# Kernel optimization log

Measured on AMD Instinct MI355X. Metric: run time of the kernel, lower is better.

The kernel has to match this reference:

```python
import jax, jax.numpy as jnp
import numpy as np

N, E = 100000, 1600000
IN_C, HID, HEADS, OUT_C = 128, 32, 4, 2
NEG_SLOPE = 0.2


def _gat_layer(x, src, dst, W, a_src, a_dst, b, n_nodes, heads, c):
    # x: [N, F_in] -> h: [N, H, C]
    h = (x @ W).reshape(n_nodes, heads, c)
    alpha_s = jnp.sum(h * a_src, axis=-1)  # [N, H]
    alpha_d = jnp.sum(h * a_dst, axis=-1)  # [N, H]
    e = jax.nn.leaky_relu(alpha_s[src] + alpha_d[dst], NEG_SLOPE)  # [E, H]
    # segment softmax over incoming edges of each dst node
    m = jax.ops.segment_max(e, dst, num_segments=n_nodes)  # [N, H]
    ee = jnp.exp(e - m[dst])
    denom = jax.ops.segment_sum(ee, dst, num_segments=n_nodes)  # [N, H]
    alpha = ee / (denom[dst] + 1e-16)  # [E, H]
    out = jax.ops.segment_sum(h[src] * alpha[:, :, None], dst, num_segments=n_nodes)  # [N, H, C]
    return out.reshape(n_nodes, heads * c) + b


def _gat_forward(x, edge_index, W1, a_src1, a_dst1, b1, W2, a_src2, a_dst2, b2, Wfc, bfc):
    n = x.shape[0]
    loops = jnp.arange(n, dtype=edge_index.dtype)
    src = jnp.concatenate([edge_index[0], loops])  # PyG adds self-loops
    dst = jnp.concatenate([edge_index[1], loops])
    h = jax.nn.elu(_gat_layer(x, src, dst, W1, a_src1, a_dst1, b1, n, HEADS, HID))
    h = jax.nn.elu(_gat_layer(h, src, dst, W2, a_src2, a_dst2, b2, n, HEADS, HID))
    return h @ Wfc + bfc


def setup_inputs() -> dict:
    key = jax.random.key(0)
    ks = jax.random.split(key, 12)
    g = lambda k, shape, fan: jax.random.normal(k, shape, jnp.float32) * (1.0 / np.sqrt(fan))
    return {
        "x": jax.random.normal(ks[0], (N, IN_C), jnp.float32),
        "edge_index": jax.random.randint(ks[1], (2, E), 0, N, jnp.int64),
        "W1": g(ks[2], (IN_C, HEADS * HID), IN_C),
        "a_src1": g(ks[3], (HEADS, HID), HID),
        "a_dst1": g(ks[4], (HEADS, HID), HID),
        "b1": jnp.zeros((HEADS * HID,), jnp.float32),
        "W2": g(ks[5], (HEADS * HID, HEADS * HID), HEADS * HID),
        "a_src2": g(ks[6], (HEADS, HID), HID),
        "a_dst2": g(ks[7], (HEADS, HID), HID),
        "b2": jnp.zeros((HEADS * HID,), jnp.float32),
        "Wfc": g(ks[8], (HEADS * HID, OUT_C), HEADS * HID),
        "bfc": jnp.zeros((OUT_C,), jnp.float32),
    }


def reference(x, edge_index, W1, a_src1, a_dst1, b1, W2, a_src2, a_dst2, b2, Wfc, bfc):
    return _gat_forward(x, edge_index, W1, a_src1, a_dst1, b1, W2, a_src2, a_dst2, b2, Wfc, bfc)
```

## Files before the change

### kernel.cpp

```cpp
#include <hip/hip_runtime.h>
#include <hip/hip_fp16.h>
#include <math.h>

#define FEAT 128
#define NBLK 256
#define BSHIFT 8

typedef _Float16 f16x8 __attribute__((ext_vector_type(8)));
typedef float f32x4 __attribute__((ext_vector_type(4)));

__device__ __forceinline__ float eluf(float x) {
  return x > 0.0f ? x : (__expf(x) - 1.0f);
}


__global__ __launch_bounds__(256) void scan1_kernel(const int* __restrict__ cnt,
                                                    int* __restrict__ pre,
                                                    int* __restrict__ bsum, int n) {
  __shared__ int sd[256];
  const int t = threadIdx.x;
  const int idx = blockIdx.x * 1024 + t * 4;
  int4 v = make_int4(0, 0, 0, 0);
  if (idx + 3 < n) {
    v = *(const int4*)(cnt + idx);
  } else {
    if (idx < n)     v.x = cnt[idx];
    if (idx + 1 < n) v.y = cnt[idx + 1];
    if (idx + 2 < n) v.z = cnt[idx + 2];
    if (idx + 3 < n) v.w = cnt[idx + 3];
  }
  const int tsum = v.x + v.y + v.z + v.w;
  sd[t] = tsum;
  __syncthreads();
  for (int o = 1; o < 256; o <<= 1) {
    int x = (t >= o) ? sd[t - o] : 0;
    __syncthreads();
    sd[t] += x;
    __syncthreads();
  }
  const int excl = sd[t] - tsum;
  if (idx < n)     pre[idx]     = excl;
  if (idx + 1 < n) pre[idx + 1] = excl + v.x;
  if (idx + 2 < n) pre[idx + 2] = excl + v.x + v.y;
  if (idx + 3 < n) pre[idx + 3] = excl + v.x + v.y + v.z;
  if (t == 255) bsum[blockIdx.x] = sd[255];
}

__global__ __launch_bounds__(256) void scan2_kernel(int* __restrict__ bsum, int nb) {
  __shared__ int sd[256];
  const int t = threadIdx.x;
  int v = (t < nb) ? bsum[t] : 0;
  sd[t] = v;
  __syncthreads();
  for (int o = 1; o < 256; o <<= 1) {
    int x = (t >= o) ? sd[t - o] : 0;
    __syncthreads();
    sd[t] += x;
    __syncthreads();
  }
  if (t < nb) bsum[t] = sd[t] - v;
}

__global__ __launch_bounds__(256) void bucket_hist_kernel(
    const int* __restrict__ ei, int* __restrict__ gh,
    int E, int ET, int nbuck, int chunk) {
  __shared__ int h[512];
  const int t = threadIdx.x;
  const int b = blockIdx.x;
  h[t] = 0; h[t + 256] = 0;
  __syncthreads();
  const int lo = b * chunk;
  const int hi = min(lo + chunk, ET);
  for (int i = lo + t; i < hi; i += 256) {
    int d = (i < E) ? ei[E + i] : (i - E);
    atomicAdd(&h[d >> BSHIFT], 1);
  }
  __syncthreads();
  for (int k = t; k < nbuck; k += 256) gh[k * NBLK + b] = h[k];
}

__global__ __launch_bounds__(256) void bucket_scatter_kernel(
    const int* __restrict__ ei, const int* __restrict__ ghp,
    const int* __restrict__ bsum, unsigned* __restrict__ pairs,
    int E, int ET, int nbuck, int chunk) {
  __shared__ int cur[512];
  const int t = threadIdx.x;
  const int b = blockIdx.x;
  for (int k = t; k < nbuck; k += 256) {
    int idx = k * NBLK + b;
    cur[k] = ghp[idx] + bsum[idx >> 10];
  }
  __syncthreads();
  const int lo = b * chunk;
  const int hi = min(lo + chunk, ET);
  for (int i = lo + t; i < hi; i += 256) {
    int s, d;
    if (i < E) { s = ei[i]; d = ei[E + i]; } else { s = d = i - E; }
    int pos = atomicAdd(&cur[d >> BSHIFT], 1);
    pairs[pos] = ((unsigned)s << 8) | (unsigned)(d & 255);
  }
}

__global__ __launch_bounds__(256) void bucket_finalize_kernel(
    const unsigned* __restrict__ pairs, const int* __restrict__ ghp,
    const int* __restrict__ bsum, int* __restrict__ row_ptr,
    int* __restrict__ esrc, int N, int ET, int nbuck) {
  __shared__ int hist[256];
  __shared__ int cur[256];
  __shared__ int sd[256];
  const int t = threadIdx.x;
  const int k = blockIdx.x;
  const int node0 = k << BSHIFT;
  const int idx0 = k * NBLK;
  const int base = ghp[idx0] + bsum[idx0 >> 10];
  int end;
  if (k + 1 < nbuck) {
    const int idx1 = (k + 1) * NBLK;
    end = ghp[idx1] + bsum[idx1 >> 10];
  } else {
    end = ET;
  }
  hist[t] = 0;
  __syncthreads();
  for (int e = base + t; e < end; e += 256) {
    atomicAdd(&hist[pairs[e] & 255u], 1);
  }
  __syncthreads();
  const int v = hist[t];
  __syncthreads();
  sd[t] = v;
  __syncthreads();
  for (int o = 1; o < 256; o <<= 1) {
    int x = (t >= o) ? sd[t - o] : 0;
    __syncthreads();
    sd[t] += x;
    __syncthreads();
  }
  const int excl = sd[t] - v;
  if (node0 + t < N) row_ptr[node0 + t] = base + excl;
  cur[t] = excl;
  __syncthreads();
  for (int e = base + t; e < end; e += 256) {
    unsigned p = pairs[e];
    int pos = atomicAdd(&cur[p & 255u], 1);
    esrc[base + pos] = (int)(p >> 8);
  }
  if (k == 0 && t == 0) row_ptr[N] = ET;
}

__global__ __launch_bounds__(256) void pack_w_kernel(
    const float* __restrict__ W, const float* __restrict__ a_src,
    const float* __restrict__ a_dst, __half* __restrict__ frag) {
  const float LOG2E = 1.4426950408889634f;
  int tid = blockIdx.x * 256 + threadIdx.x;
  if (tid >= 4 * 9 * 64) return;
  int lane = tid & 63;
  int tile = (tid >> 6) % 9;
  int ks = tid / (9 * 64);
  int li = lane & 15, hi = lane >> 4;
  int col = tile * 16 + li;
  __half* dst = frag + (size_t)tid * 8;
  for (int i = 0; i < 8; ++i) {
    int k = ks * 32 + hi * 8 + i;
    float v = 0.f;
    if (col < 128) {
      v = W[k * 128 + col];
    } else if (col < 132) {
      int h = col - 128;
      float s = 0.f;
      for (int j = 0; j < 32; ++j) s += W[k * 128 + h * 32 + j] * a_src[h * 32 + j];
      v = s * LOG2E;
    } else if (col < 136) {
      int h = col - 132;
      float s = 0.f;
      for (int j = 0; j < 32; ++j) s += W[k * 128 + h * 32 + j] * a_dst[h * 32 + j];
      v = s * LOG2E;
    }
    dst[i] = __float2half(v);
  }
}

template <bool F32IN>
__device__ __forceinline__ f16x8 load_x(const void* in, int row, int ks, int hi) {
  f16x8 xf;
  if (F32IN) {
    const float* xp = (const float*)in + (size_t)row * FEAT + ks * 32 + hi * 8;
    float4 v0 = *(const float4*)xp;
    float4 v1 = *(const float4*)(xp + 4);
    xf[0] = (_Float16)v0.x; xf[1] = (_Float16)v0.y;
    xf[2] = (_Float16)v0.z; xf[3] = (_Float16)v0.w;
    xf[4] = (_Float16)v1.x; xf[5] = (_Float16)v1.y;
    xf[6] = (_Float16)v1.z; xf[7] = (_Float16)v1.w;
  } else {
    xf = *(const f16x8*)((const __half*)in + (size_t)row * FEAT + ks * 32 + hi * 8);
  }
  return xf;
}

template <bool F32IN>
__global__ __launch_bounds__(256) void gemm_mfma_kernel(
    const void* __restrict__ in, const __half* __restrict__ frag,
    __half* __restrict__ hout, float* __restrict__ as_out, float* __restrict__ ad_out,
    int nrows) {
  const int wv = (blockIdx.x * 256 + threadIdx.x) >> 6;
  const int lane = threadIdx.x & 63;
  const int li = lane & 15, hi = lane >> 4;
  const int ntiles = (nrows + 15) >> 4;
  const int t0 = wv * 2;
  if (t0 >= ntiles) return;

  int row0 = t0 * 16 + li;
  int row1 = row0 + 16;
  const bool v0 = row0 < nrows;
  const bool v1 = (t0 + 1 < ntiles) && (row1 < nrows);
  const int r0 = v0 ? row0 : nrows - 1;
  const int r1 = v1 ? row1 : nrows - 1;

  const f16x8* fragv = (const f16x8*)frag;

  f32x4 acc0[9], acc1[9];
#pragma unroll
  for (int t = 0; t < 9; ++t) {
    acc0[t] = (f32x4){0.f, 0.f, 0.f, 0.f};
    acc1[t] = (f32x4){0.f, 0.f, 0.f, 0.f};
  }

#pragma unroll
  for (int ks = 0; ks < 4; ++ks) {
    const f16x8 xf0 = load_x<F32IN>(in, r0, ks, hi);
    const f16x8 xf1 = load_x<F32IN>(in, r1, ks, hi);
#pragma unroll
    for (int t = 0; t < 9; ++t) {
      const f16x8 wf = fragv[(ks * 9 + t) * 64 + lane];
      acc0[t] = __builtin_amdgcn_mfma_f32_16x16x32_f16(wf, xf0, acc0[t], 0, 0, 0);
      acc1[t] = __builtin_amdgcn_mfma_f32_16x16x32_f16(wf, xf1, acc1[t], 0, 0, 0);
    }
  }

  if (v0) {
#pragma unroll
    for (int t = 0; t < 8; ++t) {
      union { __half2 h[2]; uint2 u; } pk;
      pk.h[0] = __floats2half2_rn(acc0[t][0], acc0[t][1]);
      pk.h[1] = __floats2half2_rn(acc0[t][2], acc0[t][3]);
      *(uint2*)(hout + (size_t)r0 * FEAT + t * 16 + hi * 4) = pk.u;
    }
    if (hi == 0) *(float4*)(as_out + r0 * 4) = make_float4(acc0[8][0], acc0[8][1], acc0[8][2], acc0[8][3]);
    if (hi == 1) *(float4*)(ad_out + r0 * 4) = make_float4(acc0[8][0], acc0[8][1], acc0[8][2], acc0[8][3]);
  }
  if (v1) {
#pragma unroll
    for (int t = 0; t < 8; ++t) {
      union { __half2 h[2]; uint2 u; } pk;
      pk.h[0] = __floats2half2_rn(acc1[t][0], acc1[t][1]);
      pk.h[1] = __floats2half2_rn(acc1[t][2], acc1[t][3]);
      *(uint2*)(hout + (size_t)r1 * FEAT + t * 16 + hi * 4) = pk.u;
    }
    if (hi == 0) *(float4*)(as_out + r1 * 4) = make_float4(acc1[8][0], acc1[8][1], acc1[8][2], acc1[8][3]);
    if (hi == 1) *(float4*)(ad_out + r1 * 4) = make_float4(acc1[8][0], acc1[8][1], acc1[8][2], acc1[8][3]);
  }
}

template <int MODE>
__global__ __launch_bounds__(256) void node_gat_kernel(
    const int* __restrict__ row_ptr, const int* __restrict__ esrc,
    const float* __restrict__ as_, const float* __restrict__ ad_,
    const __half2* __restrict__ h, const float* __restrict__ bias,
    __half2* __restrict__ out16, const float* __restrict__ fcw,
    const float* __restrict__ fcb, float* __restrict__ outf, int n) {
  const int wid = (blockIdx.x * 256 + threadIdx.x) >> 6;
  if (wid >= n) return;
  const int l = threadIdx.x & 63;
  const int begin = row_ptr[wid];
  const int end = row_ptr[wid + 1];
  const unsigned hd = (unsigned)(l >> 4);
  const float adv = ad_[(unsigned)wid * 4u + hd];
  const unsigned lofs = (unsigned)l;

  float2 a2 = make_float2(0.f, 0.f);
  float den = 0.f;
  int e = begin;

  for (; e + 7 < end; e += 8) {
    unsigned s[8];
#pragma unroll
    for (int i = 0; i < 8; ++i) s[i] = (unsigned)esrc[e + i];
    float as8[8];
#pragma unroll
    for (int i = 0; i < 8; ++i) as8[i] = as_[s[i] * 4u + hd];
    __half2 hv[8];
#pragma unroll
    for (int i = 0; i < 8; ++i) hv[i] = h[(s[i] << 6) | lofs];
#pragma unroll
    for (int i = 0; i < 8; ++i) {
      const float x = as8[i] + adv;
      const float w = __builtin_amdgcn_exp2f(fmaxf(x, 0.2f * x));
      den += w;
      a2.x = fmaf(__half2float(hv[i].x), w, a2.x);
      a2.y = fmaf(__half2float(hv[i].y), w, a2.y);
    }
  }
  for (; e + 3 < end; e += 4) {
    unsigned s[4];
#pragma unroll
    for (int i = 0; i < 4; ++i) s[i] = (unsigned)esrc[e + i];
    float as4[4];
#pragma unroll
    for (int i = 0; i < 4; ++i) as4[i] = as_[s[i] * 4u + hd];
    __half2 hv[4];
#pragma unroll
    for (int i = 0; i < 4; ++i) hv[i] = h[(s[i] << 6) | lofs];
#pragma unroll
    for (int i = 0; i < 4; ++i) {
      const float x = as4[i] + adv;
      const float w = __builtin_amdgcn_exp2f(fmaxf(x, 0.2f * x));
      den += w;
      a2.x = fmaf(__half2float(hv[i].x), w, a2.x);
      a2.y = fmaf(__half2float(hv[i].y), w, a2.y);
    }
  }
  for (; e < end; ++e) {
    const unsigned s0 = (unsigned)esrc[e];
    const float x = as_[s0 * 4u + hd] + adv;
    const float w = __builtin_amdgcn_exp2f(fmaxf(x, 0.2f * x));
    const __half2 h0 = h[(s0 << 6) | lofs];
    den += w;
    a2.x = fmaf(__half2float(h0.x), w, a2.x);
    a2.y = fmaf(__half2float(h0.y), w, a2.y);
  }

  const float inv = 1.0f / (den + 1e-16f);
  const float o0 = a2.x * inv;
  const float o1 = a2.y * inv;
  const float2 b = *(const float2*)(bias + l * 2);
  if (MODE == 0) {
    out16[((unsigned)wid << 6) | lofs] = __floats2half2_rn(eluf(o0 + b.x), eluf(o1 + b.y));
  } else {
    const float e0 = eluf(o0 + b.x);
    const float e1 = eluf(o1 + b.y);
    const float4 w4 = *(const float4*)(fcw + l * 4);
    float s0 = e0 * w4.x + e1 * w4.z;
    float s1 = e0 * w4.y + e1 * w4.w;
#pragma unroll
    for (int o = 32; o >= 1; o >>= 1) {
      s0 += __shfl_xor(s0, o);
      s1 += __shfl_xor(s1, o);
    }
    if (l == 0) {
      *(float2*)(outf + (size_t)wid * 2) = make_float2(s0 + fcb[0], s1 + fcb[1]);
    }
  }
}

extern "C" void kernel_launch(void* const* d_in, const int* in_sizes, int n_in,
                              void* d_out, int out_size, void* d_ws, size_t ws_size,
                              hipStream_t stream) {
  const float* x   = (const float*)d_in[0];
  const int*   ei  = (const int*)d_in[1];
  const float* W1  = (const float*)d_in[2];
  const float* as1 = (const float*)d_in[3];
  const float* ad1 = (const float*)d_in[4];
  const float* b1  = (const float*)d_in[5];
  const float* W2  = (const float*)d_in[6];
  const float* as2 = (const float*)d_in[7];
  const float* ad2 = (const float*)d_in[8];
  const float* b2  = (const float*)d_in[9];
  const float* Wfc = (const float*)d_in[10];
  const float* bfc = (const float*)d_in[11];
  float* out = (float*)d_out;

  const int N = in_sizes[0] / FEAT;
  const int E = in_sizes[1] / 2;
  const int ET = E + N;
  const int nbuck = (N + 255) >> BSHIFT;
  const int NN = nbuck * NBLK;
  const int chunk = (ET + NBLK - 1) / NBLK;

  char* ws = (char*)d_ws;
  __half* hraw = (__half*)ws;
  __half* hin2 = hraw + (size_t)N * FEAT;
  float* acc   = (float*)(hin2 + (size_t)N * FEAT);
  float* asb   = acc + (size_t)N * FEAT;
  float* adb   = asb + (size_t)N * 4;
  __half* bfrag1 = (__half*)(adb + (size_t)N * 4);
  __half* bfrag2 = bfrag1 + 4 * 9 * 64 * 8;
  int* bsum    = (int*)(bfrag2 + 4 * 9 * 64 * 8);
  int* row_ptr = bsum + 256;
  int* esrc    = row_ptr + (N + 1);
  int* gh    = (int*)acc;
  int* ghp   = gh + NN;
  unsigned* pairs = (unsigned*)(ghp + NN);

  const dim3 b256(256);
  const int nb = (NN + 1023) / 1024;

  pack_w_kernel<<<9, b256, 0, stream>>>(W1, as1, ad1, bfrag1);
  pack_w_kernel<<<9, b256, 0, stream>>>(W2, as2, ad2, bfrag2);

  bucket_hist_kernel<<<NBLK, b256, 0, stream>>>(ei, gh, E, ET, nbuck, chunk);
  scan1_kernel<<<nb, b256, 0, stream>>>(gh, ghp, bsum, NN);
  scan2_kernel<<<1, b256, 0, stream>>>(bsum, nb);
  bucket_scatter_kernel<<<NBLK, b256, 0, stream>>>(ei, ghp, bsum, pairs, E, ET, nbuck, chunk);
  bucket_finalize_kernel<<<nbuck, b256, 0, stream>>>(pairs, ghp, bsum, row_ptr, esrc, N, ET, nbuck);

  const int ntiles = (N + 15) / 16;
  const int nwv = (ntiles + 1) / 2;
  const int ggrid = (nwv + 3) / 4;
  const int wgrid = (N * 64 + 255) / 256;

  gemm_mfma_kernel<true><<<ggrid, b256, 0, stream>>>(x, bfrag1, hraw, asb, adb, N);
  node_gat_kernel<0><<<wgrid, b256, 0, stream>>>(row_ptr, esrc, asb, adb,
                                                 (const __half2*)hraw, b1,
                                                 (__half2*)hin2, nullptr, nullptr, nullptr, N);

  gemm_mfma_kernel<false><<<ggrid, b256, 0, stream>>>(hin2, bfrag2, hraw, asb, adb, N);
  node_gat_kernel<1><<<wgrid, b256, 0, stream>>>(row_ptr, esrc, asb, adb,
                                                 (const __half2*)hraw, b2,
                                                 nullptr, Wfc, bfc, out, N);
}
```

Baseline: 278.3 us.

## Process two destination nodes per wavefront in layer-1 GAT aggregation

Adds a paired node aggregation kernel for layer 1, where each wavefront interleaves the edge loops of two consecutive destination nodes. This doubles the independent gather loads in flight per wave to hide memory latency. The GEMM goes back to one 16-row tile per wave, trading row reuse of weight fragments for more waves. The two weight-packing launches are merged into one. The tail loops run serially per node, so nodes with unequal degrees get less overlap, and register use rises.

```diff
diff --git a/kernel.cpp b/kernel.cpp
--- a/kernel.cpp
+++ b/kernel.cpp
@@ -149,11 +149,20 @@
 }
 
 __global__ __launch_bounds__(256) void pack_w_kernel(
-    const float* __restrict__ W, const float* __restrict__ a_src,
-    const float* __restrict__ a_dst, __half* __restrict__ frag) {
+    const float* __restrict__ W1, const float* __restrict__ as1,
+    const float* __restrict__ ad1, __half* __restrict__ frag1,
+    const float* __restrict__ W2, const float* __restrict__ as2,
+    const float* __restrict__ ad2, __half* __restrict__ frag2) {
   const float LOG2E = 1.4426950408889634f;
   int tid = blockIdx.x * 256 + threadIdx.x;
-  if (tid >= 4 * 9 * 64) return;
+  const int PER = 4 * 9 * 64;
+  if (tid >= 2 * PER) return;
+  const bool second = tid >= PER;
+  if (second) tid -= PER;
+  const float* W = second ? W2 : W1;
+  const float* a_src = second ? as2 : as1;
+  const float* a_dst = second ? ad2 : ad1;
+  __half* frag = second ? frag2 : frag1;
   int lane = tid & 63;
   int tile = (tid >> 6) % 9;
   int ks = tid / (9 * 64);
@@ -181,83 +190,107 @@
 }
 
 template <bool F32IN>
-__device__ __forceinline__ f16x8 load_x(const void* in, int row, int ks, int hi) {
-  f16x8 xf;
-  if (F32IN) {
-    const float* xp = (const float*)in + (size_t)row * FEAT + ks * 32 + hi * 8;
-    float4 v0 = *(const float4*)xp;
-    float4 v1 = *(const float4*)(xp + 4);
-    xf[0] = (_Float16)v0.x; xf[1] = (_Float16)v0.y;
-    xf[2] = (_Float16)v0.z; xf[3] = (_Float16)v0.w;
-    xf[4] = (_Float16)v1.x; xf[5] = (_Float16)v1.y;
-    xf[6] = (_Float16)v1.z; xf[7] = (_Float16)v1.w;
-  } else {
-    xf = *(const f16x8*)((const __half*)in + (size_t)row * FEAT + ks * 32 + hi * 8);
-  }
-  return xf;
-}
-
-template <bool F32IN>
 __global__ __launch_bounds__(256) void gemm_mfma_kernel(
     const void* __restrict__ in, const __half* __restrict__ frag,
     __half* __restrict__ hout, float* __restrict__ as_out, float* __restrict__ ad_out,
     int nrows) {
-  const int wv = (blockIdx.x * 256 + threadIdx.x) >> 6;
+  const int wid = (blockIdx.x * 256 + threadIdx.x) >> 6;
   const int lane = threadIdx.x & 63;
   const int li = lane & 15, hi = lane >> 4;
-  const int ntiles = (nrows + 15) >> 4;
-  const int t0 = wv * 2;
-  if (t0 >= ntiles) return;
-
-  int row0 = t0 * 16 + li;
-  int row1 = row0 + 16;
-  const bool v0 = row0 < nrows;
-  const bool v1 = (t0 + 1 < ntiles) && (row1 < nrows);
-  const int r0 = v0 ? row0 : nrows - 1;
-  const int r1 = v1 ? row1 : nrows - 1;
+  int row = wid * 16 + li;
+  const bool valid = row < nrows;
+  if (wid * 16 >= nrows) return;
+  if (!valid) row = nrows - 1;
 
   const f16x8* fragv = (const f16x8*)frag;
 
-  f32x4 acc0[9], acc1[9];
-#pragma unroll
-  for (int t = 0; t < 9; ++t) {
-    acc0[t] = (f32x4){0.f, 0.f, 0.f, 0.f};
-    acc1[t] = (f32x4){0.f, 0.f, 0.f, 0.f};
-  }
+  f32x4 acc[9];
+#pragma unroll
+  for (int t = 0; t < 9; ++t) acc[t] = (f32x4){0.f, 0.f, 0.f, 0.f};
 
 #pragma unroll
   for (int ks = 0; ks < 4; ++ks) {
-    const f16x8 xf0 = load_x<F32IN>(in, r0, ks, hi);
-    const f16x8 xf1 = load_x<F32IN>(in, r1, ks, hi);
+    f16x8 xf;
+    if (F32IN) {
+      const float* xp = (const float*)in + (size_t)row * FEAT + ks * 32 + hi * 8;
+      float4 v0 = *(const float4*)xp;
+      float4 v1 = *(const float4*)(xp + 4);
+      xf[0] = (_Float16)v0.x; xf[1] = (_Float16)v0.y;
+      xf[2] = (_Float16)v0.z; xf[3] = (_Float16)v0.w;
+      xf[4] = (_Float16)v1.x; xf[5] = (_Float16)v1.y;
+      xf[6] = (_Float16)v1.z; xf[7] = (_Float16)v1.w;
+    } else {
+      xf = *(const f16x8*)((const __half*)in + (size_t)row * FEAT + ks * 32 + hi * 8);
+    }
 #pragma unroll
     for (int t = 0; t < 9; ++t) {
-      const f16x8 wf = fragv[(ks * 9 + t) * 64 + lane];
-      acc0[t] = __builtin_amdgcn_mfma_f32_16x16x32_f16(wf, xf0, acc0[t], 0, 0, 0);
-      acc1[t] = __builtin_amdgcn_mfma_f32_16x16x32_f16(wf, xf1, acc1[t], 0, 0, 0);
-    }
-  }
-
-  if (v0) {
-#pragma unroll
-    for (int t = 0; t < 8; ++t) {
-      union { __half2 h[2]; uint2 u; } pk;
-      pk.h[0] = __floats2half2_rn(acc0[t][0], acc0[t][1]);
-      pk.h[1] = __floats2half2_rn(acc0[t][2], acc0[t][3]);
-      *(uint2*)(hout + (size_t)r0 * FEAT + t * 16 + hi * 4) = pk.u;
-    }
-    if (hi == 0) *(float4*)(as_out + r0 * 4) = make_float4(acc0[8][0], acc0[8][1], acc0[8][2], acc0[8][3]);
-    if (hi == 1) *(float4*)(ad_out + r0 * 4) = make_float4(acc0[8][0], acc0[8][1], acc0[8][2], acc0[8][3]);
-  }
-  if (v1) {
-#pragma unroll
-    for (int t = 0; t < 8; ++t) {
-      union { __half2 h[2]; uint2 u; } pk;
-      pk.h[0] = __floats2half2_rn(acc1[t][0], acc1[t][1]);
-      pk.h[1] = __floats2half2_rn(acc1[t][2], acc1[t][3]);
-      *(uint2*)(hout + (size_t)r1 * FEAT + t * 16 + hi * 4) = pk.u;
-    }
-    if (hi == 0) *(float4*)(as_out + r1 * 4) = make_float4(acc1[8][0], acc1[8][1], acc1[8][2], acc1[8][3]);
-    if (hi == 1) *(float4*)(ad_out + r1 * 4) = make_float4(acc1[8][0], acc1[8][1], acc1[8][2], acc1[8][3]);
+      f16x8 wf = fragv[(ks * 9 + t) * 64 + lane];
+      acc[t] = __builtin_amdgcn_mfma_f32_16x16x32_f16(wf, xf, acc[t], 0, 0, 0);
+    }
+  }
+
+  if (!valid) return;
+#pragma unroll
+  for (int t = 0; t < 8; ++t) {
+    union { __half2 h[2]; uint2 u; } pk;
+    pk.h[0] = __floats2half2_rn(acc[t][0], acc[t][1]);
+    pk.h[1] = __floats2half2_rn(acc[t][2], acc[t][3]);
+    *(uint2*)(hout + (size_t)row * FEAT + t * 16 + hi * 4) = pk.u;
+  }
+  if (hi == 0) *(float4*)(as_out + row * 4) = make_float4(acc[8][0], acc[8][1], acc[8][2], acc[8][3]);
+  if (hi == 1) *(float4*)(ad_out + row * 4) = make_float4(acc[8][0], acc[8][1], acc[8][2], acc[8][3]);
+}
+
+__device__ __forceinline__ void gat_accum(
+    const int* __restrict__ esrc, const float* __restrict__ as_,
+    const __half2* __restrict__ h, float adv, unsigned hd, unsigned lofs,
+    int e, int end, float2& a2, float& den) {
+  for (; e + 7 < end; e += 8) {
+    unsigned s[8];
+#pragma unroll
+    for (int i = 0; i < 8; ++i) s[i] = (unsigned)esrc[e + i];
+    float as8[8];
+#pragma unroll
+    for (int i = 0; i < 8; ++i) as8[i] = as_[s[i] * 4u + hd];
+    __half2 hv[8];
+#pragma unroll
+    for (int i = 0; i < 8; ++i) hv[i] = h[((size_t)s[i] << 6) | lofs];
+#pragma unroll
+    for (int i = 0; i < 8; ++i) {
+      const float x = as8[i] + adv;
+      const float w = __builtin_amdgcn_exp2f(fmaxf(x, 0.2f * x));
+      den += w;
+      a2.x = fmaf(__half2float(hv[i].x), w, a2.x);
+      a2.y = fmaf(__half2float(hv[i].y), w, a2.y);
+    }
+  }
+  for (; e + 3 < end; e += 4) {
+    unsigned s[4];
+#pragma unroll
+    for (int i = 0; i < 4; ++i) s[i] = (unsigned)esrc[e + i];
+    float as4[4];
+#pragma unroll
+    for (int i = 0; i < 4; ++i) as4[i] = as_[s[i] * 4u + hd];
+    __half2 hv[4];
+#pragma unroll
+    for (int i = 0; i < 4; ++i) hv[i] = h[((size_t)s[i] << 6) | lofs];
+#pragma unroll
+    for (int i = 0; i < 4; ++i) {
+      const float x = as4[i] + adv;
+      const float w = __builtin_amdgcn_exp2f(fmaxf(x, 0.2f * x));
+      den += w;
+      a2.x = fmaf(__half2float(hv[i].x), w, a2.x);
+      a2.y = fmaf(__half2float(hv[i].y), w, a2.y);
+    }
+  }
+  for (; e < end; ++e) {
+    const unsigned s0 = (unsigned)esrc[e];
+    const float x = as_[s0 * 4u + hd] + adv;
+    const float w = __builtin_amdgcn_exp2f(fmaxf(x, 0.2f * x));
+    const __half2 h0 = h[((size_t)s0 << 6) | lofs];
+    den += w;
+    a2.x = fmaf(__half2float(h0.x), w, a2.x);
+    a2.y = fmaf(__half2float(h0.y), w, a2.y);
   }
 }
 
@@ -271,70 +304,23 @@
   const int wid = (blockIdx.x * 256 + threadIdx.x) >> 6;
   if (wid >= n) return;
   const int l = threadIdx.x & 63;
+  const unsigned hd = (unsigned)(l >> 4);
+  const unsigned lofs = (unsigned)l;
   const int begin = row_ptr[wid];
   const int end = row_ptr[wid + 1];
-  const unsigned hd = (unsigned)(l >> 4);
   const float adv = ad_[(unsigned)wid * 4u + hd];
-  const unsigned lofs = (unsigned)l;
 
   float2 a2 = make_float2(0.f, 0.f);
   float den = 0.f;
-  int e = begin;
-
-  for (; e + 7 < end; e += 8) {
-    unsigned s[8];
-#pragma unroll
-    for (int i = 0; i < 8; ++i) s[i] = (unsigned)esrc[e + i];
-    float as8[8];
-#pragma unroll
-    for (int i = 0; i < 8; ++i) as8[i] = as_[s[i] * 4u + hd];
-    __half2 hv[8];
-#pragma unroll
-    for (int i = 0; i < 8; ++i) hv[i] = h[(s[i] << 6) | lofs];
-#pragma unroll
-    for (int i = 0; i < 8; ++i) {
-      const float x = as8[i] + adv;
-      const float w = __builtin_amdgcn_exp2f(fmaxf(x, 0.2f * x));
-      den += w;
-      a2.x = fmaf(__half2float(hv[i].x), w, a2.x);
-      a2.y = fmaf(__half2float(hv[i].y), w, a2.y);
-    }
-  }
-  for (; e + 3 < end; e += 4) {
-    unsigned s[4];
-#pragma unroll
-    for (int i = 0; i < 4; ++i) s[i] = (unsigned)esrc[e + i];
-    float as4[4];
-#pragma unroll
-    for (int i = 0; i < 4; ++i) as4[i] = as_[s[i] * 4u + hd];
-    __half2 hv[4];
-#pragma unroll
-    for (int i = 0; i < 4; ++i) hv[i] = h[(s[i] << 6) | lofs];
-#pragma unroll
-    for (int i = 0; i < 4; ++i) {
-      const float x = as4[i] + adv;
-      const float w = __builtin_amdgcn_exp2f(fmaxf(x, 0.2f * x));
-      den += w;
-      a2.x = fmaf(__half2float(hv[i].x), w, a2.x);
-      a2.y = fmaf(__half2float(hv[i].y), w, a2.y);
-    }
-  }
-  for (; e < end; ++e) {
-    const unsigned s0 = (unsigned)esrc[e];
-    const float x = as_[s0 * 4u + hd] + adv;
-    const float w = __builtin_amdgcn_exp2f(fmaxf(x, 0.2f * x));
-    const __half2 h0 = h[(s0 << 6) | lofs];
-    den += w;
-    a2.x = fmaf(__half2float(h0.x), w, a2.x);
-    a2.y = fmaf(__half2float(h0.y), w, a2.y);
-  }
+  gat_accum(esrc, as_, h, adv, hd, lofs, begin, end, a2, den);
 
   const float inv = 1.0f / (den + 1e-16f);
   const float o0 = a2.x * inv;
   const float o1 = a2.y * inv;
   const float2 b = *(const float2*)(bias + l * 2);
   if (MODE == 0) {
-    out16[((unsigned)wid << 6) | lofs] = __floats2half2_rn(eluf(o0 + b.x), eluf(o1 + b.y));
+    out16[((size_t)(unsigned)wid << 6) | lofs] =
+        __floats2half2_rn(eluf(o0 + b.x), eluf(o1 + b.y));
   } else {
     const float e0 = eluf(o0 + b.x);
     const float e1 = eluf(o1 + b.y);
@@ -349,6 +335,81 @@
     if (l == 0) {
       *(float2*)(outf + (size_t)wid * 2) = make_float2(s0 + fcb[0], s1 + fcb[1]);
     }
+  }
+}
+
+__global__ __launch_bounds__(256) void node_gat_pair_kernel(
+    const int* __restrict__ row_ptr, const int* __restrict__ esrc,
+    const float* __restrict__ as_, const float* __restrict__ ad_,
+    const __half2* __restrict__ h, const float* __restrict__ bias,
+    __half2* __restrict__ out16, int n) {
+  const int wpair = (blockIdx.x * 256 + threadIdx.x) >> 6;
+  const int wid0 = wpair * 2;
+  if (wid0 >= n) return;
+  const int wid1 = wid0 + 1;
+  const bool has1 = wid1 < n;
+  const int l = threadIdx.x & 63;
+  const unsigned hd = (unsigned)(l >> 4);
+  const unsigned lofs = (unsigned)l;
+
+  const int b0 = row_ptr[wid0];
+  const int m0 = row_ptr[wid0 + 1];
+  const int m1 = has1 ? row_ptr[wid1 + 1] : m0;
+  const float adv0 = ad_[(unsigned)wid0 * 4u + hd];
+  const float adv1 = has1 ? ad_[(unsigned)wid1 * 4u + hd] : 0.f;
+
+  float2 a20 = make_float2(0.f, 0.f), a21 = make_float2(0.f, 0.f);
+  float den0 = 0.f, den1 = 0.f;
+  int p0 = b0, p1 = m0;
+
+  while (p0 + 7 < m0 && p1 + 7 < m1) {
+    unsigned s0[8], s1[8];
+#pragma unroll
+    for (int i = 0; i < 8; ++i) s0[i] = (unsigned)esrc[p0 + i];
+#pragma unroll
+    for (int i = 0; i < 8; ++i) s1[i] = (unsigned)esrc[p1 + i];
+    float as0[8], as1[8];
+#pragma unroll
+    for (int i = 0; i < 8; ++i) as0[i] = as_[s0[i] * 4u + hd];
+#pragma unroll
+    for (int i = 0; i < 8; ++i) as1[i] = as_[s1[i] * 4u + hd];
+    __half2 hv0[8], hv1[8];
+#pragma unroll
+    for (int i = 0; i < 8; ++i) hv0[i] = h[((size_t)s0[i] << 6) | lofs];
+#pragma unroll
+    for (int i = 0; i < 8; ++i) hv1[i] = h[((size_t)s1[i] << 6) | lofs];
+#pragma unroll
+    for (int i = 0; i < 8; ++i) {
+      const float x = as0[i] + adv0;
+      const float w = __builtin_amdgcn_exp2f(fmaxf(x, 0.2f * x));
+      den0 += w;
+      a20.x = fmaf(__half2float(hv0[i].x), w, a20.x);
+      a20.y = fmaf(__half2float(hv0[i].y), w, a20.y);
+    }
+#pragma unroll
+    for (int i = 0; i < 8; ++i) {
+      const float x = as1[i] + adv1;
+      const float w = __builtin_amdgcn_exp2f(fmaxf(x, 0.2f * x));
+      den1 += w;
+      a21.x = fmaf(__half2float(hv1[i].x), w, a21.x);
+      a21.y = fmaf(__half2float(hv1[i].y), w, a21.y);
+    }
+    p0 += 8;
+    p1 += 8;
+  }
+  gat_accum(esrc, as_, h, adv0, hd, lofs, p0, m0, a20, den0);
+  if (has1) gat_accum(esrc, as_, h, adv1, hd, lofs, p1, m1, a21, den1);
+
+  const float2 b = *(const float2*)(bias + l * 2);
+  {
+    const float inv = 1.0f / (den0 + 1e-16f);
+    out16[((size_t)(unsigned)wid0 << 6) | lofs] =
+        __floats2half2_rn(eluf(a20.x * inv + b.x), eluf(a20.y * inv + b.y));
+  }
+  if (has1) {
+    const float inv = 1.0f / (den1 + 1e-16f);
+    out16[((size_t)(unsigned)wid1 << 6) | lofs] =
+        __floats2half2_rn(eluf(a21.x * inv + b.x), eluf(a21.y * inv + b.y));
   }
 }
 
@@ -394,8 +455,7 @@
   const dim3 b256(256);
   const int nb = (NN + 1023) / 1024;
 
-  pack_w_kernel<<<9, b256, 0, stream>>>(W1, as1, ad1, bfrag1);
-  pack_w_kernel<<<9, b256, 0, stream>>>(W2, as2, ad2, bfrag2);
+  pack_w_kernel<<<18, b256, 0, stream>>>(W1, as1, ad1, bfrag1, W2, as2, ad2, bfrag2);
 
   bucket_hist_kernel<<<NBLK, b256, 0, stream>>>(ei, gh, E, ET, nbuck, chunk);
   scan1_kernel<<<nb, b256, 0, stream>>>(gh, ghp, bsum, NN);
@@ -404,14 +464,15 @@
   bucket_finalize_kernel<<<nbuck, b256, 0, stream>>>(pairs, ghp, bsum, row_ptr, esrc, N, ET, nbuck);
 
   const int ntiles = (N + 15) / 16;
-  const int nwv = (ntiles + 1) / 2;
-  const int ggrid = (nwv + 3) / 4;
+  const int ggrid = (ntiles + 3) / 4;
+  const int npair = (N + 1) / 2;
+  const int pgrid = (npair + 3) / 4;
   const int wgrid = (N * 64 + 255) / 256;
 
   gemm_mfma_kernel<true><<<ggrid, b256, 0, stream>>>(x, bfrag1, hraw, asb, adb, N);
-  node_gat_kernel<0><<<wgrid, b256, 0, stream>>>(row_ptr, esrc, asb, adb,
-                                                 (const __half2*)hraw, b1,
-                                                 (__half2*)hin2, nullptr, nullptr, nullptr, N);
+  node_gat_pair_kernel<<<pgrid, b256, 0, stream>>>(row_ptr, esrc, asb, adb,
+                                                   (const __half2*)hraw, b1,
+                                                   (__half2*)hin2, N);
 
   gemm_mfma_kernel<false><<<ggrid, b256, 0, stream>>>(hin2, bfrag2, hraw, asb, adb, N);
   node_gat_kernel<1><<<wgrid, b256, 0, stream>>>(row_ptr, esrc, asb, adb,
```

New measurement: 268.4 us. 3.6% less time.

## Stage weight fragments in LDS and use persistent grid-stride GEMM; merge pack kernels

Applied to the files above, without the earlier changes.

The GEMM kernel now copies the packed weight fragments into shared memory once per block and runs a persistent grid-stride loop over 16-row tiles with a fixed grid of 256 blocks. Previously each wave read the fragments from global memory and did two tiles. The two weight-packing launches are merged into one, and the per-node accumulation loop is factored into a helper with size_t indexing. The fixed grid may underuse the GPU's compute units. Doing one tile per wave also removes the reuse of each weight fragment across two row tiles.

```diff
diff --git a/kernel.cpp b/kernel.cpp
--- a/kernel.cpp
+++ b/kernel.cpp
@@ -149,11 +149,20 @@
 }
 
 __global__ __launch_bounds__(256) void pack_w_kernel(
-    const float* __restrict__ W, const float* __restrict__ a_src,
-    const float* __restrict__ a_dst, __half* __restrict__ frag) {
+    const float* __restrict__ W1, const float* __restrict__ as1,
+    const float* __restrict__ ad1, __half* __restrict__ frag1,
+    const float* __restrict__ W2, const float* __restrict__ as2,
+    const float* __restrict__ ad2, __half* __restrict__ frag2) {
   const float LOG2E = 1.4426950408889634f;
   int tid = blockIdx.x * 256 + threadIdx.x;
-  if (tid >= 4 * 9 * 64) return;
+  const int PER = 4 * 9 * 64;
+  if (tid >= 2 * PER) return;
+  const bool second = tid >= PER;
+  if (second) tid -= PER;
+  const float* W = second ? W2 : W1;
+  const float* a_src = second ? as2 : as1;
+  const float* a_dst = second ? ad2 : ad1;
+  __half* frag = second ? frag2 : frag1;
   int lane = tid & 63;
   int tile = (tid >> 6) % 9;
   int ks = tid / (9 * 64);
@@ -181,83 +190,123 @@
 }
 
 template <bool F32IN>
-__device__ __forceinline__ f16x8 load_x(const void* in, int row, int ks, int hi) {
-  f16x8 xf;
-  if (F32IN) {
-    const float* xp = (const float*)in + (size_t)row * FEAT + ks * 32 + hi * 8;
-    float4 v0 = *(const float4*)xp;
-    float4 v1 = *(const float4*)(xp + 4);
-    xf[0] = (_Float16)v0.x; xf[1] = (_Float16)v0.y;
-    xf[2] = (_Float16)v0.z; xf[3] = (_Float16)v0.w;
-    xf[4] = (_Float16)v1.x; xf[5] = (_Float16)v1.y;
-    xf[6] = (_Float16)v1.z; xf[7] = (_Float16)v1.w;
-  } else {
-    xf = *(const f16x8*)((const __half*)in + (size_t)row * FEAT + ks * 32 + hi * 8);
-  }
-  return xf;
-}
-
-template <bool F32IN>
 __global__ __launch_bounds__(256) void gemm_mfma_kernel(
     const void* __restrict__ in, const __half* __restrict__ frag,
     __half* __restrict__ hout, float* __restrict__ as_out, float* __restrict__ ad_out,
     int nrows) {
-  const int wv = (blockIdx.x * 256 + threadIdx.x) >> 6;
-  const int lane = threadIdx.x & 63;
+  __shared__ __half lfrag[36 * 64 * 8];
+  const int t = threadIdx.x;
+  {
+    f16x8* lf = (f16x8*)lfrag;
+    const f16x8* gf = (const f16x8*)frag;
+#pragma unroll
+    for (int k = 0; k < 9; ++k) {
+      const int id = k * 256 + t;
+      lf[id] = gf[id];
+    }
+  }
+  __syncthreads();
+
+  const int lane = t & 63;
   const int li = lane & 15, hi = lane >> 4;
   const int ntiles = (nrows + 15) >> 4;
-  const int t0 = wv * 2;
-  if (t0 >= ntiles) return;
-
-  int row0 = t0 * 16 + li;
-  int row1 = row0 + 16;
-  const bool v0 = row0 < nrows;
-  const bool v1 = (t0 + 1 < ntiles) && (row1 < nrows);
-  const int r0 = v0 ? row0 : nrows - 1;
-  const int r1 = v1 ? row1 : nrows - 1;
-
-  const f16x8* fragv = (const f16x8*)frag;
-
-  f32x4 acc0[9], acc1[9];
-#pragma unroll
-  for (int t = 0; t < 9; ++t) {
-    acc0[t] = (f32x4){0.f, 0.f, 0.f, 0.f};
-    acc1[t] = (f32x4){0.f, 0.f, 0.f, 0.f};
-  }
-
-#pragma unroll
-  for (int ks = 0; ks < 4; ++ks) {
-    const f16x8 xf0 = load_x<F32IN>(in, r0, ks, hi);
-    const f16x8 xf1 = load_x<F32IN>(in, r1, ks, hi);
-#pragma unroll
-    for (int t = 0; t < 9; ++t) {
-      const f16x8 wf = fragv[(ks * 9 + t) * 64 + lane];
-      acc0[t] = __builtin_amdgcn_mfma_f32_16x16x32_f16(wf, xf0, acc0[t], 0, 0, 0);
-      acc1[t] = __builtin_amdgcn_mfma_f32_16x16x32_f16(wf, xf1, acc1[t], 0, 0, 0);
-    }
-  }
-
-  if (v0) {
-#pragma unroll
-    for (int t = 0; t < 8; ++t) {
-      union { __half2 h[2]; uint2 u; } pk;
-      pk.h[0] = __floats2half2_rn(acc0[t][0], acc0[t][1]);
-      pk.h[1] = __floats2half2_rn(acc0[t][2], acc0[t][3]);
-      *(uint2*)(hout + (size_t)r0 * FEAT + t * 16 + hi * 4) = pk.u;
-    }
-    if (hi == 0) *(float4*)(as_out + r0 * 4) = make_float4(acc0[8][0], acc0[8][1], acc0[8][2], acc0[8][3]);
-    if (hi == 1) *(float4*)(ad_out + r0 * 4) = make_float4(acc0[8][0], acc0[8][1], acc0[8][2], acc0[8][3]);
-  }
-  if (v1) {
-#pragma unroll
-    for (int t = 0; t < 8; ++t) {
-      union { __half2 h[2]; uint2 u; } pk;
-      pk.h[0] = __floats2half2_rn(acc1[t][0], acc1[t][1]);
-      pk.h[1] = __floats2half2_rn(acc1[t][2], acc1[t][3]);
-      *(uint2*)(hout + (size_t)r1 * FEAT + t * 16 + hi * 4) = pk.u;
-    }
-    if (hi == 0) *(float4*)(as_out + r1 * 4) = make_float4(acc1[8][0], acc1[8][1], acc1[8][2], acc1[8][3]);
-    if (hi == 1) *(float4*)(ad_out + r1 * 4) = make_float4(acc1[8][0], acc1[8][1], acc1[8][2], acc1[8][3]);
+  const int nwaves = gridDim.x << 2;
+  const f16x8* lf = (const f16x8*)lfrag;
+
+  for (int tile = (blockIdx.x * 256 + t) >> 6; tile < ntiles; tile += nwaves) {
+    int row = tile * 16 + li;
+    const bool valid = row < nrows;
+    const int r = valid ? row : nrows - 1;
+
+    f32x4 acc[9];
+#pragma unroll
+    for (int q = 0; q < 9; ++q) acc[q] = (f32x4){0.f, 0.f, 0.f, 0.f};
+
+#pragma unroll
+    for (int ks = 0; ks < 4; ++ks) {
+      f16x8 xf;
+      if (F32IN) {
+        const float* xp = (const float*)in + (size_t)r * FEAT + ks * 32 + hi * 8;
+        float4 v0 = *(const float4*)xp;
+        float4 v1 = *(const float4*)(xp + 4);
+        xf[0] = (_Float16)v0.x; xf[1] = (_Float16)v0.y;
+        xf[2] = (_Float16)v0.z; xf[3] = (_Float16)v0.w;
+        xf[4] = (_Float16)v1.x; xf[5] = (_Float16)v1.y;
+        xf[6] = (_Float16)v1.z; xf[7] = (_Float16)v1.w;
+      } else {
+        xf = *(const f16x8*)((const __half*)in + (size_t)r * FEAT + ks * 32 + hi * 8);
+      }
+#pragma unroll
+      for (int q = 0; q < 9; ++q) {
+        const f16x8 wf = lf[(ks * 9 + q) * 64 + lane];
+        acc[q] = __builtin_amdgcn_mfma_f32_16x16x32_f16(wf, xf, acc[q], 0, 0, 0);
+      }
+    }
+
+    if (valid) {
+#pragma unroll
+      for (int q = 0; q < 8; ++q) {
+        union { __half2 h[2]; uint2 u; } pk;
+        pk.h[0] = __floats2half2_rn(acc[q][0], acc[q][1]);
+        pk.h[1] = __floats2half2_rn(acc[q][2], acc[q][3]);
+        *(uint2*)(hout + (size_t)r * FEAT + q * 16 + hi * 4) = pk.u;
+      }
+      if (hi == 0) *(float4*)(as_out + r * 4) = make_float4(acc[8][0], acc[8][1], acc[8][2], acc[8][3]);
+      if (hi == 1) *(float4*)(ad_out + r * 4) = make_float4(acc[8][0], acc[8][1], acc[8][2], acc[8][3]);
+    }
+  }
+}
+
+__device__ __forceinline__ void gat_accum(
+    const int* __restrict__ esrc, const float* __restrict__ as_,
+    const __half2* __restrict__ h, float adv, unsigned hd, unsigned lofs,
+    int e, int end, float2& a2, float& den) {
+  for (; e + 7 < end; e += 8) {
+    unsigned s[8];
+#pragma unroll
+    for (int i = 0; i < 8; ++i) s[i] = (unsigned)esrc[e + i];
+    float as8[8];
+#pragma unroll
+    for (int i = 0; i < 8; ++i) as8[i] = as_[s[i] * 4u + hd];
+    __half2 hv[8];
+#pragma unroll
+    for (int i = 0; i < 8; ++i) hv[i] = h[((size_t)s[i] << 6) | lofs];
+#pragma unroll
+    for (int i = 0; i < 8; ++i) {
+      const float x = as8[i] + adv;
+      const float w = __builtin_amdgcn_exp2f(fmaxf(x, 0.2f * x));
+      den += w;
+      a2.x = fmaf(__half2float(hv[i].x), w, a2.x);
+      a2.y = fmaf(__half2float(hv[i].y), w, a2.y);
+    }
+  }
+  for (; e + 3 < end; e += 4) {
+    unsigned s[4];
+#pragma unroll
+    for (int i = 0; i < 4; ++i) s[i] = (unsigned)esrc[e + i];
+    float as4[4];
+#pragma unroll
+    for (int i = 0; i < 4; ++i) as4[i] = as_[s[i] * 4u + hd];
+    __half2 hv[4];
+#pragma unroll
+    for (int i = 0; i < 4; ++i) hv[i] = h[((size_t)s[i] << 6) | lofs];
+#pragma unroll
+    for (int i = 0; i < 4; ++i) {
+      const float x = as4[i] + adv;
+      const float w = __builtin_amdgcn_exp2f(fmaxf(x, 0.2f * x));
+      den += w;
+      a2.x = fmaf(__half2float(hv[i].x), w, a2.x);
+      a2.y = fmaf(__half2float(hv[i].y), w, a2.y);
+    }
+  }
+  for (; e < end; ++e) {
+    const unsigned s0 = (unsigned)esrc[e];
+    const float x = as_[s0 * 4u + hd] + adv;
+    const float w = __builtin_amdgcn_exp2f(fmaxf(x, 0.2f * x));
+    const __half2 h0 = h[((size_t)s0 << 6) | lofs];
+    den += w;
+    a2.x = fmaf(__half2float(h0.x), w, a2.x);
+    a2.y = fmaf(__half2float(h0.y), w, a2.y);
   }
 }
 
@@ -271,70 +320,23 @@
   const int wid = (blockIdx.x * 256 + threadIdx.x) >> 6;
   if (wid >= n) return;
   const int l = threadIdx.x & 63;
+  const unsigned hd = (unsigned)(l >> 4);
+  const unsigned lofs = (unsigned)l;
   const int begin = row_ptr[wid];
   const int end = row_ptr[wid + 1];
-  const unsigned hd = (unsigned)(l >> 4);
   const float adv = ad_[(unsigned)wid * 4u + hd];
-  const unsigned lofs = (unsigned)l;
 
   float2 a2 = make_float2(0.f, 0.f);
   float den = 0.f;
-  int e = begin;
-
-  for (; e + 7 < end; e += 8) {
-    unsigned s[8];
-#pragma unroll
-    for (int i = 0; i < 8; ++i) s[i] = (unsigned)esrc[e + i];
-    float as8[8];
-#pragma unroll
-    for (int i = 0; i < 8; ++i) as8[i] = as_[s[i] * 4u + hd];
-    __half2 hv[8];
-#pragma unroll
-    for (int i = 0; i < 8; ++i) hv[i] = h[(s[i] << 6) | lofs];
-#pragma unroll
-    for (int i = 0; i < 8; ++i) {
-      const float x = as8[i] + adv;
-      const float w = __builtin_amdgcn_exp2f(fmaxf(x, 0.2f * x));
-      den += w;
-      a2.x = fmaf(__half2float(hv[i].x), w, a2.x);
-      a2.y = fmaf(__half2float(hv[i].y), w, a2.y);
-    }
-  }
-  for (; e + 3 < end; e += 4) {
-    unsigned s[4];
-#pragma unroll
-    for (int i = 0; i < 4; ++i) s[i] = (unsigned)esrc[e + i];
-    float as4[4];
-#pragma unroll
-    for (int i = 0; i < 4; ++i) as4[i] = as_[s[i] * 4u + hd];
-    __half2 hv[4];
-#pragma unroll
-    for (int i = 0; i < 4; ++i) hv[i] = h[(s[i] << 6) | lofs];
-#pragma unroll
-    for (int i = 0; i < 4; ++i) {
-      const float x = as4[i] + adv;
-      const float w = __builtin_amdgcn_exp2f(fmaxf(x, 0.2f * x));
-      den += w;
-      a2.x = fmaf(__half2float(hv[i].x), w, a2.x);
-      a2.y = fmaf(__half2float(hv[i].y), w, a2.y);
-    }
-  }
-  for (; e < end; ++e) {
-    const unsigned s0 = (unsigned)esrc[e];
-    const float x = as_[s0 * 4u + hd] + adv;
-    const float w = __builtin_amdgcn_exp2f(fmaxf(x, 0.2f * x));
-    const __half2 h0 = h[(s0 << 6) | lofs];
-    den += w;
-    a2.x = fmaf(__half2float(h0.x), w, a2.x);
-    a2.y = fmaf(__half2float(h0.y), w, a2.y);
-  }
+  gat_accum(esrc, as_, h, adv, hd, lofs, begin, end, a2, den);
 
   const float inv = 1.0f / (den + 1e-16f);
   const float o0 = a2.x * inv;
   const float o1 = a2.y * inv;
   const float2 b = *(const float2*)(bias + l * 2);
   if (MODE == 0) {
-    out16[((unsigned)wid << 6) | lofs] = __floats2half2_rn(eluf(o0 + b.x), eluf(o1 + b.y));
+    out16[((size_t)(unsigned)wid << 6) | lofs] =
+        __floats2half2_rn(eluf(o0 + b.x), eluf(o1 + b.y));
   } else {
     const float e0 = eluf(o0 + b.x);
     const float e1 = eluf(o1 + b.y);
@@ -394,8 +396,7 @@
   const dim3 b256(256);
   const int nb = (NN + 1023) / 1024;
 
-  pack_w_kernel<<<9, b256, 0, stream>>>(W1, as1, ad1, bfrag1);
-  pack_w_kernel<<<9, b256, 0, stream>>>(W2, as2, ad2, bfrag2);
+  pack_w_kernel<<<18, b256, 0, stream>>>(W1, as1, ad1, bfrag1, W2, as2, ad2, bfrag2);
 
   bucket_hist_kernel<<<NBLK, b256, 0, stream>>>(ei, gh, E, ET, nbuck, chunk);
   scan1_kernel<<<nb, b256, 0, stream>>>(gh, ghp, bsum, NN);
@@ -403,9 +404,7 @@
   bucket_scatter_kernel<<<NBLK, b256, 0, stream>>>(ei, ghp, bsum, pairs, E, ET, nbuck, chunk);
   bucket_finalize_kernel<<<nbuck, b256, 0, stream>>>(pairs, ghp, bsum, row_ptr, esrc, N, ET, nbuck);
 
-  const int ntiles = (N + 15) / 16;
-  const int nwv = (ntiles + 1) / 2;
-  const int ggrid = (nwv + 3) / 4;
+  const int ggrid = 256;
   const int wgrid = (N * 64 + 255) / 256;
 
   gemm_mfma_kernel<true><<<ggrid, b256, 0, stream>>>(x, bfrag1, hraw, asb, adb, N);
```

After: 248.5 us. -10.7%, faster.
